# Kernel tuning notes

Measured on AMD Instinct MI355X. Metric: run time of the kernel, lower is better.

## Reference

```python
import jax, jax.numpy as jnp
import numpy as np

B_DIM = 64        # block_dim
IN_DIM = 4096     # input_dim = block_dim**2
HE = 2            # hidden_expansion
HID = IN_DIM * HE # 8192
STRIDE0 = B_DIM * HE  # 128


def setup_inputs() -> dict:
    key = jax.random.key(0)
    ks = jax.random.split(key, 5)
    x = jax.random.normal(ks[0], (8192, IN_DIM), dtype=jnp.float32)
    # BlockLinear weights, matching torch.randn init
    w0 = jax.random.normal(ks[1], (IN_DIM // B_DIM, B_DIM, B_DIM * HE), dtype=jnp.float32)   # (64,64,128)
    w1 = jax.random.normal(ks[2], (HID // B_DIM, B_DIM, B_DIM), dtype=jnp.float32)           # (128,64,64)
    b1 = jnp.zeros((HID // B_DIM, 1, B_DIM), dtype=jnp.float32)                               # (128,1,64)
    w2 = jax.random.normal(ks[3], (HID // B_DIM, B_DIM, B_DIM), dtype=jnp.float32)           # (128,64,64)
    w3 = jax.random.normal(ks[4], (IN_DIM // B_DIM, B_DIM * HE, B_DIM), dtype=jnp.float32)   # (64,128,64)
    b3 = jnp.zeros((IN_DIM // B_DIM, 1, B_DIM), dtype=jnp.float32)                            # (64,1,64)
    return {"x": x, "w0": w0, "w1": w1, "b1": b1, "w2": w2, "w3": w3, "b3": b3}


def reference(x, w0, w1, b1, w2, w3, b3):
    bs = x.shape[0]
    # stage 0_0: view(bs, 64, 64); blocks over first reshaped axis; no bias
    y = x.reshape(bs, IN_DIM // B_DIM, B_DIM)                    # (B,64,64)
    y = jnp.einsum('bnk,nkh->bnh', y, w0)                        # (B,64,128)
    # stage 0_1: flat view(bs, 64, 128), permute so blocks over last axis (stride0)
    y = jnp.einsum('bks,skj->bsj', y, w1) + b1[:, 0, :]          # (B,128,64)
    y = jax.nn.elu(y.reshape(bs, HID)).reshape(bs, HID // B_DIM, B_DIM)
    # stage 1_0: blocks over first reshaped axis; no bias
    y = jnp.einsum('bnk,nkj->bnj', y, w2)                        # (B,128,64)
    # stage 1_1: flat view(bs, 128, 64), permute so blocks over last axis
    y = jnp.einsum('bks,skj->bsj', y, w3) + b3[:, 0, :]          # (B,64,64)
    return y.reshape(bs, IN_DIM)
```

## Files before the change

### kernel.cpp

```cpp
#include <hip/hip_runtime.h>


typedef __attribute__((ext_vector_type(8))) short short8;
typedef __attribute__((ext_vector_type(4))) float floatx4;
typedef unsigned int uint;
typedef unsigned short ushort;

#define MFMA32(a, b, c) __builtin_amdgcn_mfma_f32_16x16x32_bf16(a, b, c, 0, 0, 0)

__device__ __forceinline__ ushort f2bf(float f) {
    uint u = __float_as_uint(f);
    uint r = 0x7FFFu + ((u >> 16) & 1u);
    return (ushort)((u + r) >> 16);
}
__device__ __forceinline__ short8 ld8(const ushort* p) {
    return *reinterpret_cast<const short8*>(p);
}
__device__ __forceinline__ void gload_lds16(const void* g, void* l) {
    __builtin_amdgcn_global_load_lds(
        (const __attribute__((address_space(1))) unsigned int*)g,
        (__attribute__((address_space(3))) unsigned int*)l, 16, 0, 0);
}
__device__ __forceinline__ void lgkm_barrier() {
    __builtin_amdgcn_sched_barrier(0);
    asm volatile("s_waitcnt lgkmcnt(0)" ::: "memory");
    __builtin_amdgcn_s_barrier();
    __builtin_amdgcn_sched_barrier(0);
}

__global__ void prep_weights(const float* __restrict__ w0, const float* __restrict__ w1,
                             const float* __restrict__ w2, const float* __restrict__ w3,
                             ushort* __restrict__ w0s, ushort* __restrict__ w1t,
                             ushort* __restrict__ w2t, ushort* __restrict__ w3s) {
    int stride = gridDim.x * blockDim.x;
    for (int idx = blockIdx.x * blockDim.x + threadIdx.x; idx < 4 * 524288; idx += stride) {
        const int seg = idx >> 19;
        const int local = idx & 524287;
        const float* in; ushort* out; int R, C; bool swz;
        if (seg == 0)      { in = w0; out = w0s; R = 64;  C = 128; swz = true;  }
        else if (seg == 1) { in = w1; out = w1t; R = 64;  C = 64;  swz = false; }
        else if (seg == 2) { in = w2; out = w2t; R = 64;  C = 64;  swz = false; }
        else               { in = w3; out = w3s; R = 128; C = 64;  swz = true;  }
        const int rc = R * C;
        const int b = local / rc;
        const int rem = local - b * rc;
        const int c = rem / R;
        const int r = rem - c * R;
        const ushort v = f2bf(in[(size_t)(b * R + r) * C + c]);
        if (swz) {
            int byteoff = ((c * R + r) * 2) ^ ((c & 7) << 4);
            *reinterpret_cast<ushort*>((char*)out + (size_t)b * rc * 2 + byteoff) = v;
        } else {
            out[local] = v;
        }
    }
}


__global__ __launch_bounds__(512, 2) void pass1_k(
    const float* __restrict__ x,
    const ushort* __restrict__ w0s,
    ushort* __restrict__ y0t)
{
    const int tid = threadIdx.x, lane = tid & 63, wv = tid >> 6;
    const int l15 = lane & 15, l4 = lane >> 4;
    const int slice = blockIdx.x & 7;
    const int r0 = (blockIdx.x >> 3) * 128;
    const int p   = wv & 3;
    const int st0 = (wv >> 2) * 4;

    __shared__ __align__(16) ushort lds[65536];
    {
        const ushort* src = w0s + (size_t)slice * 8 * 8192;
        for (int i = 0; i < 16; ++i)
            gload_lds16(src + i * 4096 + tid * 8, &lds[i * 4096 + tid * 8]);
    }
    __syncthreads();

    short8 wb[2][4][2];
    const char* wp = (const char*)lds;
#pragma unroll
    for (int kk = 0; kk < 2; ++kk)
#pragma unroll
        for (int si = 0; si < 4; ++si)
#pragma unroll
            for (int mh = 0; mh < 2; ++mh) {
                const int s = (st0 + si) * 16 + l15;
                const int byteoff = (2 * p + kk) * 16384 +
                    (((s * 64 + mh * 32 + l4 * 8) * 2) ^ ((s & 7) << 4));
                wb[kk][si][mh] = *reinterpret_cast<const short8*>(wp + byteoff);
            }
    __syncthreads();
    char* sb = (char*)lds;

    for (int rt = 0; rt < 8; ++rt) {
        short8 a[2][2];
        const float* xr = x + (size_t)(r0 + rt * 16 + l15) * 4096
                            + (slice * 8 + 2 * p) * 64;
#pragma unroll
        for (int kk = 0; kk < 2; ++kk)
#pragma unroll
            for (int mh = 0; mh < 2; ++mh) {
                const float* q = xr + kk * 64 + mh * 32 + l4 * 8;
                floatx4 u0 = *reinterpret_cast<const floatx4*>(q);
                floatx4 u1 = *reinterpret_cast<const floatx4*>(q + 4);
                short8 v;
#pragma unroll
                for (int i2 = 0; i2 < 4; ++i2) {
                    v[i2]     = (short)f2bf(u0[i2]);
                    v[i2 + 4] = (short)f2bf(u1[i2]);
                }
                a[kk][mh] = v;
            }
#pragma unroll
        for (int si = 0; si < 4; ++si) {
            floatx4 d0 = (floatx4){0.f, 0.f, 0.f, 0.f};
            floatx4 d1 = (floatx4){0.f, 0.f, 0.f, 0.f};
            d0 = MFMA32(a[0][0], wb[0][si][0], d0);
            d0 = MFMA32(a[0][1], wb[0][si][1], d0);
            d1 = MFMA32(a[1][0], wb[1][si][0], d1);
            d1 = MFMA32(a[1][1], wb[1][si][1], d1);
            const int s = (st0 + si) * 16 + l15;
#pragma unroll
            for (int rg = 0; rg < 4; ++rg) {
                const int r = l4 * 4 + rg;
                uint pk = (uint)f2bf(d0[rg]) | ((uint)f2bf(d1[rg]) << 16);
                *reinterpret_cast<uint*>(
                    sb + r * 2048 + ((s * 16 + p * 4) ^ ((r & 7) << 4))) = pk;
            }
        }
        __syncthreads();
#pragma unroll
        for (int q2 = 0; q2 < 4; ++q2) {
            const int idx = q2 * 512 + tid;
            const int row = idx >> 7, c = idx & 127;
            short8 v = *reinterpret_cast<const short8*>(
                sb + row * 2048 + ((c * 16) ^ ((row & 7) << 4)));
            *reinterpret_cast<short8*>(
                y0t + (size_t)(r0 + rt * 16 + row) * 8192 + slice * 1024 + c * 8) = v;
        }
        __syncthreads();
    }
}

__global__ __launch_bounds__(512, 4) void pass23_k(
    const ushort* __restrict__ y0t,
    const ushort* __restrict__ w1t,
    const ushort* __restrict__ w2t,
    const float* __restrict__ b1,
    ushort* __restrict__ y2t)
{
    const int tid = threadIdx.x, lane = tid & 63, wv = tid >> 6;
    const int l15 = lane & 15, l4 = lane >> 4;
    const int sblk = blockIdx.x & 15;
    const int r0 = (blockIdx.x >> 4) * 128;
    const int s = sblk * 8 + wv;

    __shared__ __align__(16) ushort zst[8 * 1024];
    __shared__ __align__(16) ushort sbuf[16 * 512];
    char* zb = (char*)zst + wv * 2048;

    short8 wbf[4][2], wc[4][2];
    float bvv[4];
#pragma unroll
    for (int jq = 0; jq < 4; ++jq) {
#pragma unroll
        for (int kh = 0; kh < 2; ++kh) {
            wbf[jq][kh] = ld8(w1t + ((size_t)s * 64 + jq * 16 + l15) * 64
                                  + kh * 32 + l4 * 8);
            wc[jq][kh]  = ld8(w2t + ((size_t)s * 64 + jq * 16 + l15) * 64
                                  + kh * 32 + l4 * 8);
        }
        bvv[jq] = b1[s * 64 + jq * 16 + l15];
    }

    const ushort* abase = y0t + (size_t)(r0 + l15) * 8192 + l4 * 1024 + s * 8;
    short8 a0 = ld8(abase), a1 = ld8(abase + 4096);

    for (int rt = 0; rt < 8; ++rt) {
#pragma unroll
        for (int jq = 0; jq < 4; ++jq) {
            floatx4 t = (floatx4){0.f, 0.f, 0.f, 0.f};
            t = MFMA32(a0, wbf[jq][0], t);
            t = MFMA32(a1, wbf[jq][1], t);
#pragma unroll
            for (int rg = 0; rg < 4; ++rg) {
                float v = t[rg] + bvv[jq];
                v = v > 0.f ? v : (__expf(v) - 1.f);
                const int r = l4 * 4 + rg;
                *reinterpret_cast<ushort*>(
                    zb + ((r * 128 + (jq * 16 + l15) * 2) ^ ((r & 7) << 4))) = f2bf(v);
            }
        }
        __builtin_amdgcn_sched_barrier(0);
        asm volatile("s_waitcnt lgkmcnt(0)" ::: "memory");
        __builtin_amdgcn_sched_barrier(0);

        short8 za0 = *reinterpret_cast<const short8*>(
            zb + ((l15 * 128 + l4 * 16) ^ ((l15 & 7) << 4)));
        short8 za1 = *reinterpret_cast<const short8*>(
            zb + ((l15 * 128 + 64 + l4 * 16) ^ ((l15 & 7) << 4)));
        floatx4 acc[4];
#pragma unroll
        for (int jq = 0; jq < 4; ++jq) {
            floatx4 t = (floatx4){0.f, 0.f, 0.f, 0.f};
            t = MFMA32(za0, wc[jq][0], t);
            t = MFMA32(za1, wc[jq][1], t);
            acc[jq] = t;
        }

        if (rt + 1 < 8) {
            const ushort* ap = abase + (size_t)(rt + 1) * 16 * 8192;
            a0 = ld8(ap);
            a1 = ld8(ap + 4096);
        }

#pragma unroll
        for (int jq = 0; jq < 4; ++jq)
#pragma unroll
            for (int rg = 0; rg < 4; ++rg) {
                const int r = l4 * 4 + rg;
                *reinterpret_cast<ushort*>(
                    (char*)sbuf + r * 1024 + (jq * 16 + l15) * 16 + wv * 2) =
                    f2bf(acc[jq][rg]);
            }
        lgkm_barrier();
#pragma unroll
        for (int q2 = 0; q2 < 2; ++q2) {
            const int idx = q2 * 512 + tid;
            const int row = idx >> 6, c = idx & 63;
            short8 v = *reinterpret_cast<const short8*>(
                (char*)sbuf + row * 1024 + c * 16);
            *reinterpret_cast<short8*>(
                y2t + (size_t)(r0 + rt * 16 + row) * 8192 + sblk * 512 + c * 8) = v;
        }
        lgkm_barrier();
    }
}

__global__ __launch_bounds__(512, 2) void pass4_k(
    const ushort* __restrict__ y2t,
    const ushort* __restrict__ w3s,
    const float* __restrict__ b3,
    float* __restrict__ out)
{
    const int tid = threadIdx.x, lane = tid & 63, wv = tid >> 6;
    const int l15 = lane & 15, l4 = lane >> 4;
    const int slice = blockIdx.x & 7;
    const int r0 = (blockIdx.x >> 3) * 128;
    const int s = slice * 8 + wv;

    __shared__ __align__(16) ushort wlds[8 * 8192];
    {
        const ushort* src = w3s + (size_t)slice * 65536;
        for (int i = 0; i < 16; ++i)
            gload_lds16(src + i * 4096 + tid * 8, &wlds[i * 4096 + tid * 8]);
    }
    __syncthreads();

    short8 wb[4][4];
    const char* wp = (const char*)wlds + wv * 16384;
#pragma unroll
    for (int jq = 0; jq < 4; ++jq)
#pragma unroll
        for (int kq = 0; kq < 4; ++kq) {
            const int byteoff =
                (((jq * 16 + l15) * 128 + kq * 32 + l4 * 8) * 2) ^ ((l15 & 7) << 4);
            wb[jq][kq] = *reinterpret_cast<const short8*>(wp + byteoff);
        }

    for (int rt = 0; rt < 8; ++rt) {
        short8 a[4];
#pragma unroll
        for (int kq = 0; kq < 4; ++kq)
            a[kq] = ld8(y2t + (size_t)(r0 + rt * 16 + l15) * 8192
                            + (kq * 4 + l4) * 512 + s * 8);
        floatx4 acc[4];
#pragma unroll
        for (int jq = 0; jq < 4; ++jq) acc[jq] = (floatx4){0.f, 0.f, 0.f, 0.f};
#pragma unroll
        for (int kq = 0; kq < 4; ++kq)
#pragma unroll
            for (int jq = 0; jq < 4; ++jq)
                acc[jq] = MFMA32(a[kq], wb[jq][kq], acc[jq]);
#pragma unroll
        for (int jq = 0; jq < 4; ++jq) {
            const float bv = b3[s * 64 + jq * 16 + l15];
#pragma unroll
            for (int rg = 0; rg < 4; ++rg)
                out[(size_t)(r0 + rt * 16 + l4 * 4 + rg) * 4096
                    + s * 64 + jq * 16 + l15] = acc[jq][rg] + bv;
        }
    }
}

extern "C" void kernel_launch(void* const* d_in, const int* in_sizes, int n_in,
                              void* d_out, int out_size, void* d_ws, size_t ws_size,
                              hipStream_t stream) {
    const float* x  = (const float*)d_in[0];
    const float* w0 = (const float*)d_in[1];
    const float* w1 = (const float*)d_in[2];
    const float* b1 = (const float*)d_in[3];
    const float* w2 = (const float*)d_in[4];
    const float* w3 = (const float*)d_in[5];
    const float* b3 = (const float*)d_in[6];
    float* out = (float*)d_out;

    const int bs = in_sizes[0] / 4096;

    ushort* y2t2 = (ushort*)d_ws;
    const size_t zElems = (size_t)bs * 8192;
    ushort* w0s = y2t2 + zElems;
    ushort* w1t = w0s + 64 * 128 * 64;
    ushort* w2t = w1t + 128 * 64 * 64;
    ushort* w3s = w2t + 128 * 64 * 64;
    const size_t need = (zElems + 4ull * 524288) * sizeof(ushort);
    if (n_in < 7 || (bs & 127) || ws_size < need) return;

    ushort* y0t = (ushort*)d_out;

    prep_weights<<<dim3(1024), dim3(256), 0, stream>>>(
        w0, w1, w2, w3, w0s, w1t, w2t, w3s);

    pass1_k <<<dim3((bs / 128) * 8),  dim3(512), 0, stream>>>(x, w0s, y0t);
    pass23_k<<<dim3((bs / 128) * 16), dim3(512), 0, stream>>>(y0t, w1t, w2t, b1, y2t2);
    pass4_k <<<dim3((bs / 128) * 8),  dim3(512), 0, stream>>>(y2t2, w3s, b3, out);
}
```

Baseline: 228.4 us.

## Split pass1 and pass4 work across twice as many blocks with half LDS

Pass1 now splits each slice's 128 output columns across two blocks, and pass4 splits slices over 16 blocks with waves sharing a slice across two output halves. Each block stages half as much weight into LDS, allowing more resident blocks per CU and a larger grid. The trade-off is that pass1 re-reads the fp32 input rows once per half, and pass4 waves redundantly load the same activation fragments.

New measurement: 286.0 us. 25.2% more time.

```diff
diff --git a/kernel.cpp b/kernel.cpp
--- a/kernel.cpp
+++ b/kernel.cpp
@@ -65,29 +65,30 @@
     const int tid = threadIdx.x, lane = tid & 63, wv = tid >> 6;
     const int l15 = lane & 15, l4 = lane >> 4;
     const int slice = blockIdx.x & 7;
-    const int r0 = (blockIdx.x >> 3) * 128;
+    const int shalf = (blockIdx.x >> 3) & 1;
+    const int r0 = (blockIdx.x >> 4) * 128;
     const int p   = wv & 3;
-    const int st0 = (wv >> 2) * 4;
-
-    __shared__ __align__(16) ushort lds[65536];
+    const int st0 = (wv >> 2) * 2;
+
+    __shared__ __align__(16) ushort lds[32768];
     {
-        const ushort* src = w0s + (size_t)slice * 8 * 8192;
-        for (int i = 0; i < 16; ++i)
-            gload_lds16(src + i * 4096 + tid * 8, &lds[i * 4096 + tid * 8]);
+        for (int i = 0; i < 8; ++i)
+            gload_lds16(w0s + (size_t)(slice * 8 + i) * 8192 + shalf * 4096 + tid * 8,
+                        &lds[i * 4096 + tid * 8]);
     }
     __syncthreads();
 
-    short8 wb[2][4][2];
+    short8 wb[2][2][2];
     const char* wp = (const char*)lds;
 #pragma unroll
     for (int kk = 0; kk < 2; ++kk)
 #pragma unroll
-        for (int si = 0; si < 4; ++si)
+        for (int si = 0; si < 2; ++si)
 #pragma unroll
             for (int mh = 0; mh < 2; ++mh) {
-                const int s = (st0 + si) * 16 + l15;
-                const int byteoff = (2 * p + kk) * 16384 +
-                    (((s * 64 + mh * 32 + l4 * 8) * 2) ^ ((s & 7) << 4));
+                const int s_l = (st0 + si) * 16 + l15;
+                const int byteoff = (2 * p + kk) * 8192 +
+                    (((s_l * 64 + mh * 32 + l4 * 8) * 2) ^ ((s_l & 7) << 4));
                 wb[kk][si][mh] = *reinterpret_cast<const short8*>(wp + byteoff);
             }
     __syncthreads();
@@ -113,31 +114,32 @@
                 a[kk][mh] = v;
             }
 #pragma unroll
-        for (int si = 0; si < 4; ++si) {
+        for (int si = 0; si < 2; ++si) {
             floatx4 d0 = (floatx4){0.f, 0.f, 0.f, 0.f};
             floatx4 d1 = (floatx4){0.f, 0.f, 0.f, 0.f};
             d0 = MFMA32(a[0][0], wb[0][si][0], d0);
             d0 = MFMA32(a[0][1], wb[0][si][1], d0);
             d1 = MFMA32(a[1][0], wb[1][si][0], d1);
             d1 = MFMA32(a[1][1], wb[1][si][1], d1);
-            const int s = (st0 + si) * 16 + l15;
+            const int s_l = (st0 + si) * 16 + l15;
 #pragma unroll
             for (int rg = 0; rg < 4; ++rg) {
                 const int r = l4 * 4 + rg;
                 uint pk = (uint)f2bf(d0[rg]) | ((uint)f2bf(d1[rg]) << 16);
                 *reinterpret_cast<uint*>(
-                    sb + r * 2048 + ((s * 16 + p * 4) ^ ((r & 7) << 4))) = pk;
+                    sb + r * 1024 + ((s_l * 16 + p * 4) ^ ((r & 7) << 4))) = pk;
             }
         }
         __syncthreads();
 #pragma unroll
-        for (int q2 = 0; q2 < 4; ++q2) {
+        for (int q2 = 0; q2 < 2; ++q2) {
             const int idx = q2 * 512 + tid;
-            const int row = idx >> 7, c = idx & 127;
+            const int row = idx >> 6, c = idx & 63;
             short8 v = *reinterpret_cast<const short8*>(
-                sb + row * 2048 + ((c * 16) ^ ((row & 7) << 4)));
+                sb + row * 1024 + ((c * 16) ^ ((row & 7) << 4)));
             *reinterpret_cast<short8*>(
-                y0t + (size_t)(r0 + rt * 16 + row) * 8192 + slice * 1024 + c * 8) = v;
+                y0t + (size_t)(r0 + rt * 16 + row) * 8192
+                    + slice * 1024 + shalf * 512 + c * 8) = v;
         }
         __syncthreads();
     }
@@ -246,27 +248,30 @@
 {
     const int tid = threadIdx.x, lane = tid & 63, wv = tid >> 6;
     const int l15 = lane & 15, l4 = lane >> 4;
-    const int slice = blockIdx.x & 7;
-    const int r0 = (blockIdx.x >> 3) * 128;
-    const int s = slice * 8 + wv;
-
-    __shared__ __align__(16) ushort wlds[8 * 8192];
+    const int slice = blockIdx.x & 15;
+    const int r0 = (blockIdx.x >> 4) * 128;
+    const int sq = wv & 3;
+    const int jh = wv >> 2;
+    const int s = slice * 4 + sq;
+
+    __shared__ __align__(16) ushort wlds[4 * 8192];
     {
-        const ushort* src = w3s + (size_t)slice * 65536;
-        for (int i = 0; i < 16; ++i)
+        const ushort* src = w3s + (size_t)slice * 4 * 8192;
+        for (int i = 0; i < 8; ++i)
             gload_lds16(src + i * 4096 + tid * 8, &wlds[i * 4096 + tid * 8]);
     }
     __syncthreads();
 
-    short8 wb[4][4];
-    const char* wp = (const char*)wlds + wv * 16384;
-#pragma unroll
-    for (int jq = 0; jq < 4; ++jq)
+    short8 wb[2][4];
+    const char* wp = (const char*)wlds + sq * 16384;
+#pragma unroll
+    for (int jq2 = 0; jq2 < 2; ++jq2)
 #pragma unroll
         for (int kq = 0; kq < 4; ++kq) {
+            const int j = (jh * 2 + jq2) * 16 + l15;
             const int byteoff =
-                (((jq * 16 + l15) * 128 + kq * 32 + l4 * 8) * 2) ^ ((l15 & 7) << 4);
-            wb[jq][kq] = *reinterpret_cast<const short8*>(wp + byteoff);
+                ((j * 128 + kq * 32 + l4 * 8) * 2) ^ ((l15 & 7) << 4);
+            wb[jq2][kq] = *reinterpret_cast<const short8*>(wp + byteoff);
         }
 
     for (int rt = 0; rt < 8; ++rt) {
@@ -275,21 +280,22 @@
         for (int kq = 0; kq < 4; ++kq)
             a[kq] = ld8(y2t + (size_t)(r0 + rt * 16 + l15) * 8192
                             + (kq * 4 + l4) * 512 + s * 8);
-        floatx4 acc[4];
-#pragma unroll
-        for (int jq = 0; jq < 4; ++jq) acc[jq] = (floatx4){0.f, 0.f, 0.f, 0.f};
+        floatx4 acc[2];
+#pragma unroll
+        for (int jq2 = 0; jq2 < 2; ++jq2) acc[jq2] = (floatx4){0.f, 0.f, 0.f, 0.f};
 #pragma unroll
         for (int kq = 0; kq < 4; ++kq)
 #pragma unroll
-            for (int jq = 0; jq < 4; ++jq)
-                acc[jq] = MFMA32(a[kq], wb[jq][kq], acc[jq]);
-#pragma unroll
-        for (int jq = 0; jq < 4; ++jq) {
-            const float bv = b3[s * 64 + jq * 16 + l15];
+            for (int jq2 = 0; jq2 < 2; ++jq2)
+                acc[jq2] = MFMA32(a[kq], wb[jq2][kq], acc[jq2]);
+#pragma unroll
+        for (int jq2 = 0; jq2 < 2; ++jq2) {
+            const int j0 = (jh * 2 + jq2) * 16 + l15;
+            const float bv = b3[s * 64 + j0];
 #pragma unroll
             for (int rg = 0; rg < 4; ++rg)
                 out[(size_t)(r0 + rt * 16 + l4 * 4 + rg) * 4096
-                    + s * 64 + jq * 16 + l15] = acc[jq][rg] + bv;
+                    + s * 64 + j0] = acc[jq2][rg] + bv;
         }
     }
 }
@@ -322,7 +328,7 @@
     prep_weights<<<dim3(1024), dim3(256), 0, stream>>>(
         w0, w1, w2, w3, w0s, w1t, w2t, w3s);
 
-    pass1_k <<<dim3((bs / 128) * 8),  dim3(512), 0, stream>>>(x, w0s, y0t);
+    pass1_k <<<dim3((bs / 128) * 16), dim3(512), 0, stream>>>(x, w0s, y0t);
     pass23_k<<<dim3((bs / 128) * 16), dim3(512), 0, stream>>>(y0t, w1t, w2t, b1, y2t2);
-    pass4_k <<<dim3((bs / 128) * 8),  dim3(512), 0, stream>>>(y2t2, w3s, b3, out);
-}
+    pass4_k <<<dim3((bs / 128) * 16), dim3(512), 0, stream>>>(y2t2, w3s, b3, out);
+}
```

## Restructure pass1 to stage x tiles in LDS and load weights directly

Applied to the files above, without the earlier changes.

Pass1 now reads its w0 fragments straight from global memory into registers, using an unswizzled transposed layout, instead of staging 128KB of weights through LDS. Each wave converts one row-slab of x to bf16 into a small double-buffered LDS tile shared across waves. Each wave computes 8 block outputs per row and writes them packed directly to global, which removes the LDS transpose round trip and one barrier per iteration. The much smaller LDS footprint allows launch bounds of 4 blocks per CU, at the cost of more register pressure.

Measured after the change: 220.3 us. 1.04x faster.

```diff
diff --git a/kernel.cpp b/kernel.cpp
--- a/kernel.cpp
+++ b/kernel.cpp
@@ -30,14 +30,14 @@
 
 __global__ void prep_weights(const float* __restrict__ w0, const float* __restrict__ w1,
                              const float* __restrict__ w2, const float* __restrict__ w3,
-                             ushort* __restrict__ w0s, ushort* __restrict__ w1t,
+                             ushort* __restrict__ w0t, ushort* __restrict__ w1t,
                              ushort* __restrict__ w2t, ushort* __restrict__ w3s) {
     int stride = gridDim.x * blockDim.x;
     for (int idx = blockIdx.x * blockDim.x + threadIdx.x; idx < 4 * 524288; idx += stride) {
         const int seg = idx >> 19;
         const int local = idx & 524287;
         const float* in; ushort* out; int R, C; bool swz;
-        if (seg == 0)      { in = w0; out = w0s; R = 64;  C = 128; swz = true;  }
+        if (seg == 0)      { in = w0; out = w0t; R = 64;  C = 128; swz = false; }
         else if (seg == 1) { in = w1; out = w1t; R = 64;  C = 64;  swz = false; }
         else if (seg == 2) { in = w2; out = w2t; R = 64;  C = 64;  swz = false; }
         else               { in = w3; out = w3s; R = 128; C = 64;  swz = true;  }
@@ -57,89 +57,70 @@
 }
 
 
-__global__ __launch_bounds__(512, 2) void pass1_k(
+__global__ __launch_bounds__(512, 4) void pass1_k(
     const float* __restrict__ x,
-    const ushort* __restrict__ w0s,
+    const ushort* __restrict__ w0t,
     ushort* __restrict__ y0t)
 {
     const int tid = threadIdx.x, lane = tid & 63, wv = tid >> 6;
     const int l15 = lane & 15, l4 = lane >> 4;
     const int slice = blockIdx.x & 7;
     const int r0 = (blockIdx.x >> 3) * 128;
-    const int p   = wv & 3;
-    const int st0 = (wv >> 2) * 4;
-
-    __shared__ __align__(16) ushort lds[65536];
-    {
-        const ushort* src = w0s + (size_t)slice * 8 * 8192;
-        for (int i = 0; i < 16; ++i)
-            gload_lds16(src + i * 4096 + tid * 8, &lds[i * 4096 + tid * 8]);
-    }
-    __syncthreads();
-
-    short8 wb[2][4][2];
-    const char* wp = (const char*)lds;
-#pragma unroll
-    for (int kk = 0; kk < 2; ++kk)
-#pragma unroll
-        for (int si = 0; si < 4; ++si)
-#pragma unroll
-            for (int mh = 0; mh < 2; ++mh) {
-                const int s = (st0 + si) * 16 + l15;
-                const int byteoff = (2 * p + kk) * 16384 +
-                    (((s * 64 + mh * 32 + l4 * 8) * 2) ^ ((s & 7) << 4));
-                wb[kk][si][mh] = *reinterpret_cast<const short8*>(wp + byteoff);
+
+    __shared__ __align__(16) ushort xs[2][16][528];
+
+    short8 wb[8][2];
+#pragma unroll
+    for (int kb = 0; kb < 8; ++kb)
+#pragma unroll
+        for (int kh = 0; kh < 2; ++kh)
+            wb[kb][kh] = ld8(w0t + ((size_t)(slice * 8 + kb) * 128 + wv * 16 + l15) * 64
+                                 + kh * 32 + l4 * 8);
+
+    const int lrow = lane >> 2;
+    const int cq   = lane & 3;
+
+    for (int rt = 0; rt < 8; ++rt) {
+        {
+            const float* xp = x + (size_t)(r0 + rt * 16 + lrow) * 4096
+                                + (slice * 8 + wv) * 64 + cq * 16;
+            floatx4 u0 = *reinterpret_cast<const floatx4*>(xp);
+            floatx4 u1 = *reinterpret_cast<const floatx4*>(xp + 4);
+            floatx4 u2 = *reinterpret_cast<const floatx4*>(xp + 8);
+            floatx4 u3 = *reinterpret_cast<const floatx4*>(xp + 12);
+            short8 v0, v1;
+#pragma unroll
+            for (int i = 0; i < 4; ++i) {
+                v0[i]     = (short)f2bf(u0[i]);
+                v0[i + 4] = (short)f2bf(u1[i]);
+                v1[i]     = (short)f2bf(u2[i]);
+                v1[i + 4] = (short)f2bf(u3[i]);
             }
-    __syncthreads();
-    char* sb = (char*)lds;
-
-    for (int rt = 0; rt < 8; ++rt) {
-        short8 a[2][2];
-        const float* xr = x + (size_t)(r0 + rt * 16 + l15) * 4096
-                            + (slice * 8 + 2 * p) * 64;
-#pragma unroll
-        for (int kk = 0; kk < 2; ++kk)
-#pragma unroll
-            for (int mh = 0; mh < 2; ++mh) {
-                const float* q = xr + kk * 64 + mh * 32 + l4 * 8;
-                floatx4 u0 = *reinterpret_cast<const floatx4*>(q);
-                floatx4 u1 = *reinterpret_cast<const floatx4*>(q + 4);
-                short8 v;
-#pragma unroll
-                for (int i2 = 0; i2 < 4; ++i2) {
-                    v[i2]     = (short)f2bf(u0[i2]);
-                    v[i2 + 4] = (short)f2bf(u1[i2]);
-                }
-                a[kk][mh] = v;
-            }
-#pragma unroll
-        for (int si = 0; si < 4; ++si) {
-            floatx4 d0 = (floatx4){0.f, 0.f, 0.f, 0.f};
-            floatx4 d1 = (floatx4){0.f, 0.f, 0.f, 0.f};
-            d0 = MFMA32(a[0][0], wb[0][si][0], d0);
-            d0 = MFMA32(a[0][1], wb[0][si][1], d0);
-            d1 = MFMA32(a[1][0], wb[1][si][0], d1);
-            d1 = MFMA32(a[1][1], wb[1][si][1], d1);
-            const int s = (st0 + si) * 16 + l15;
-#pragma unroll
-            for (int rg = 0; rg < 4; ++rg) {
-                const int r = l4 * 4 + rg;
-                uint pk = (uint)f2bf(d0[rg]) | ((uint)f2bf(d1[rg]) << 16);
-                *reinterpret_cast<uint*>(
-                    sb + r * 2048 + ((s * 16 + p * 4) ^ ((r & 7) << 4))) = pk;
-            }
-        }
-        __syncthreads();
-#pragma unroll
-        for (int q2 = 0; q2 < 4; ++q2) {
-            const int idx = q2 * 512 + tid;
-            const int row = idx >> 7, c = idx & 127;
-            short8 v = *reinterpret_cast<const short8*>(
-                sb + row * 2048 + ((c * 16) ^ ((row & 7) << 4)));
+            ushort* dst = &xs[rt & 1][lrow][wv * 64 + cq * 16];
+            *reinterpret_cast<short8*>(dst)     = v0;
+            *reinterpret_cast<short8*>(dst + 8) = v1;
+        }
+        lgkm_barrier();
+
+        floatx4 d[8];
+#pragma unroll
+        for (int kb = 0; kb < 8; ++kb) {
+            short8 a0 = ld8(&xs[rt & 1][l15][kb * 64 + l4 * 8]);
+            short8 a1 = ld8(&xs[rt & 1][l15][kb * 64 + 32 + l4 * 8]);
+            floatx4 t = (floatx4){0.f, 0.f, 0.f, 0.f};
+            t = MFMA32(a0, wb[kb][0], t);
+            t = MFMA32(a1, wb[kb][1], t);
+            d[kb] = t;
+        }
+#pragma unroll
+        for (int rg = 0; rg < 4; ++rg) {
+            short8 pk;
+#pragma unroll
+            for (int kb = 0; kb < 8; ++kb) pk[kb] = (short)f2bf(d[kb][rg]);
             *reinterpret_cast<short8*>(
-                y0t + (size_t)(r0 + rt * 16 + row) * 8192 + slice * 1024 + c * 8) = v;
-        }
-        __syncthreads();
+                y0t + (size_t)(r0 + rt * 16 + l4 * 4 + rg) * 8192
+                    + slice * 1024 + (wv * 16 + l15) * 8) = pk;
+        }
     }
 }
 
@@ -310,8 +291,8 @@
 
     ushort* y2t2 = (ushort*)d_ws;
     const size_t zElems = (size_t)bs * 8192;
-    ushort* w0s = y2t2 + zElems;
-    ushort* w1t = w0s + 64 * 128 * 64;
+    ushort* w0t = y2t2 + zElems;
+    ushort* w1t = w0t + 64 * 128 * 64;
     ushort* w2t = w1t + 128 * 64 * 64;
     ushort* w3s = w2t + 128 * 64 * 64;
     const size_t need = (zElems + 4ull * 524288) * sizeof(ushort);
@@ -320,9 +301,9 @@
     ushort* y0t = (ushort*)d_out;
 
     prep_weights<<<dim3(1024), dim3(256), 0, stream>>>(
-        w0, w1, w2, w3, w0s, w1t, w2t, w3s);
-
-    pass1_k <<<dim3((bs / 128) * 8),  dim3(512), 0, stream>>>(x, w0s, y0t);
+        w0, w1, w2, w3, w0t, w1t, w2t, w3s);
+
+    pass1_k <<<dim3((bs / 128) * 8),  dim3(512), 0, stream>>>(x, w0t, y0t);
     pass23_k<<<dim3((bs / 128) * 16), dim3(512), 0, stream>>>(y0t, w1t, w2t, b1, y2t2);
     pass4_k <<<dim3((bs / 128) * 8),  dim3(512), 0, stream>>>(y2t2, w3s, b3, out);
 }
```
